# Performance work log

Hardware: AMD Instinct MI355X
Metric: run time of the kernel (lower is better)

The kernel has to match this reference:

```python
import jax, jax.numpy as jnp
import numpy as np

EPS = 1e-5

def _ln(x, g, b):
    mu = jnp.mean(x, axis=-1, keepdims=True)
    var = jnp.var(x, axis=-1, keepdims=True)
    return (x - mu) * jax.lax.rsqrt(var + EPS) * g + b

def setup_inputs() -> dict:
    key = jax.random.key(0)
    ks = jax.random.split(key, 12)
    T, B, D, H = 64, 2048, 512, 512
    seq = jax.random.normal(ks[0], (T, B, D), dtype=jnp.float32)
    ts = jnp.sort(jax.random.uniform(ks[1], (B, T), dtype=jnp.float32) * 10.0, axis=1)
    def xavier(k, shape):
        fan_in, fan_out = shape[1], shape[0]
        lim = float(np.sqrt(6.0 / (fan_in + fan_out)))
        return jax.random.uniform(k, shape, jnp.float32, -lim, lim)
    Wr = xavier(ks[2], (H, D + H)); br = jnp.ones((H,), jnp.float32)   # reset bias init 1.0
    Wz = xavier(ks[3], (H, D + H)); bz = jnp.ones((H,), jnp.float32)   # update bias init 1.0
    Wc = xavier(ks[4], (H, D + H)); bc = jnp.zeros((H,), jnp.float32)
    Wo = xavier(ks[5], (H, H));     bo = jnp.zeros((H,), jnp.float32)  # output projection
    gx = jnp.ones((D,), jnp.float32); bx = jnp.zeros((D,), jnp.float32)  # layer_norm_x
    gh = jnp.ones((H,), jnp.float32); bh = jnp.zeros((H,), jnp.float32)  # layer_norm_h
    gc = jnp.ones((H,), jnp.float32); bcell = jnp.zeros((H,), jnp.float32)  # layer_norm_out (cell)
    gf = jnp.ones((H,), jnp.float32); bf = jnp.zeros((H,), jnp.float32)  # final layer_norm
    return {"seq": seq, "time_stamps": ts,
            "Wr": Wr, "br": br, "Wz": Wz, "bz": bz, "Wc": Wc, "bc": bc,
            "Wo": Wo, "bo": bo, "gx": gx, "bx": bx, "gh": gh, "bh": bh,
            "gc": gc, "bcell": bcell, "gf": gf, "bf": bf}

def _cell(xn, hn, Wr, br, Wz, bz, Wc, bc, gc, bcell):
    # xn: normalized input [B,D]; hn: (normalized, time-scaled) hidden [B,H]
    xh = jnp.concatenate([xn, hn], axis=-1)
    r = jax.nn.sigmoid(xh @ Wr.T + br)
    z = jax.nn.sigmoid(xh @ Wz.T + bz)
    xrh = jnp.concatenate([xn, r * hn], axis=-1)
    h_tilde = jnp.tanh(xrh @ Wc.T + bc)
    h_new = (1.0 - z) * hn + z * h_tilde
    return _ln(h_new, gc, bcell)  # cell output layer norm (dropout is identity in eval)

def reference(seq, time_stamps, Wr, br, Wz, bz, Wc, bc, Wo, bo, gx, bx, gh, bh, gc, bcell, gf, bf):
    T, B, D = seq.shape
    # first step: h is None -> zeros, no LN on h, no time-decay
    x0 = _ln(seq[0], gx, bx)
    h0 = _cell(x0, jnp.zeros((B, Wr.shape[0]), seq.dtype), Wr, br, Wz, bz, Wc, bc, gc, bcell)
    # remaining steps under scan with LN(h) and exp(-dt) decay
    dts = (time_stamps[:, 1:] - time_stamps[:, :-1]).T  # [T-1, B]
    def step(h, inp):
        x_t, dt = inp
        xn = _ln(x_t, gx, bx)
        hn = _ln(h, gh, bh) * jnp.exp(-jnp.clip(dt, 0.0, 10.0))[:, None]
        h_new = _cell(xn, hn, Wr, br, Wz, bz, Wc, bc, gc, bcell)
        return h_new, h_new
    _, rest = jax.lax.scan(step, h0, (seq[1:], dts))
    states = jnp.concatenate([h0[None], rest], axis=0)  # [T,B,H]
    out = jnp.einsum('tbh,oh->tbo', states, Wo) + bo
    out = out + seq  # residual (input_dim == hidden_dim); dropout identity in eval
    return _ln(out, gf, bf)
```

## Files before the change

### kernel.cpp

```cpp
#include <hip/hip_runtime.h>
#include <math.h>

#define TT 64
#define BB 2048

using f32x4   = __attribute__((ext_vector_type(4))) float;
using short8  = __attribute__((ext_vector_type(8))) short;
using short4v = __attribute__((ext_vector_type(4))) short;

__device__ __forceinline__ unsigned short f2bf(float f) {
    unsigned u = __float_as_uint(f);
    u += 0x7FFF + ((u >> 16) & 1);
    return (unsigned short)(u >> 16);
}
__device__ __forceinline__ float bf2f(unsigned short h) {
    return __uint_as_float(((unsigned)h) << 16);
}
__device__ __forceinline__ float sigmoidf_(float v) { return 1.0f / (1.0f + expf(-v)); }
__device__ __forceinline__ float tanhf_(float v)    { return 1.0f - 2.0f / (expf(2.0f * v) + 1.0f); }

__global__ __launch_bounds__(256)
void cvt_kernel(const float* __restrict__ src, unsigned short* __restrict__ dst, int n) {
    int i = blockIdx.x * 256 + threadIdx.x;
    if (i < n) dst[i] = f2bf(src[i]);
}

__global__ __launch_bounds__(256)
void pack_w2(const float* __restrict__ src, unsigned short* __restrict__ dst,
             int N, int Ksrc, int kbeg, int Kpk) {
    int i = blockIdx.x * 256 + threadIdx.x;
    if (i >= N * Kpk) return;
    int n = i / Kpk, k = i - n * Kpk;
    int dstIdx = ((n >> 4) * (Kpk >> 5) + (k >> 5)) * 512 + (((k >> 3) & 3) * 16 + (n & 15)) * 8 + (k & 7);
    dst[dstIdx] = f2bf(src[(size_t)n * Ksrc + kbeg + k]);
}

__device__ __forceinline__ int pk_idx(int row, int col) {
    int ks = col >> 5, khi = (col >> 3) & 3, j = col & 7;
    return ((ks * 64) + khi * 16 + row) * 8 + j;
}

__device__ __forceinline__ void ln_row_pk(const float* __restrict__ xr,
                                          const float* __restrict__ g,
                                          const float* __restrict__ b,
                                          unsigned short* __restrict__ tile,
                                          int row, int lane) {
    const int c0 = lane * 8;
    float4 v0 = *(const float4*)(xr + c0);
    float4 v1 = *(const float4*)(xr + c0 + 4);
    float s  = v0.x + v0.y + v0.z + v0.w + v1.x + v1.y + v1.z + v1.w;
    float ss = v0.x*v0.x + v0.y*v0.y + v0.z*v0.z + v0.w*v0.w
             + v1.x*v1.x + v1.y*v1.y + v1.z*v1.z + v1.w*v1.w;
#pragma unroll
    for (int m = 32; m > 0; m >>= 1) { s += __shfl_xor(s, m); ss += __shfl_xor(ss, m); }
    const float mean = s * (1.0f / 512.0f);
    const float var  = ss * (1.0f / 512.0f) - mean * mean;
    const float rs   = rsqrtf(var + 1e-5f);
    float4 g0 = *(const float4*)(g + c0);
    float4 g1 = *(const float4*)(g + c0 + 4);
    float4 b0 = *(const float4*)(b + c0);
    float4 b1 = *(const float4*)(b + c0 + 4);
    short8 o;
    o[0] = (short)f2bf((v0.x - mean) * rs * g0.x + b0.x);
    o[1] = (short)f2bf((v0.y - mean) * rs * g0.y + b0.y);
    o[2] = (short)f2bf((v0.z - mean) * rs * g0.z + b0.z);
    o[3] = (short)f2bf((v0.w - mean) * rs * g0.w + b0.w);
    o[4] = (short)f2bf((v1.x - mean) * rs * g1.x + b1.x);
    o[5] = (short)f2bf((v1.y - mean) * rs * g1.y + b1.y);
    o[6] = (short)f2bf((v1.z - mean) * rs * g1.z + b1.z);
    o[7] = (short)f2bf((v1.w - mean) * rs * g1.w + b1.w);
    *(short8*)&tile[(((lane >> 2) * 64) + (lane & 3) * 16 + row) * 8] = o;
}

__global__ __launch_bounds__(512)
void gx_kernel(const float* __restrict__ seq, const float* __restrict__ gxw,
               const float* __restrict__ bxw, const unsigned short* __restrict__ Wx3,
               unsigned short* __restrict__ gx)
{
    __shared__ unsigned short xt[4 * 8192];
    const int tid  = threadIdx.x;
    const int w    = tid >> 6;
    const int lane = tid & 63;
    const size_t m0 = (size_t)blockIdx.x * 64;
    const int t    = (int)(m0 >> 11);
    const int bloc = (int)((m0 & 2047) >> 4);

#pragma unroll
    for (int rr = 0; rr < 8; ++rr) {
        const int r = w * 8 + rr;
        ln_row_pk(seq + (m0 + r) * 512, gxw, bxw, xt + (r >> 4) * 8192, r & 15, lane);
    }
    __syncthreads();

    for (int nt = 0; nt < 3; ++nt) {
        f32x4 acc[4][4] = {};
#pragma unroll 4
        for (int ks = 0; ks < 16; ++ks) {
            short8 a[4], b[4];
#pragma unroll
            for (int mf = 0; mf < 4; ++mf)
                a[mf] = *(const short8*)&xt[mf * 8192 + (ks * 64 + lane) * 8];
#pragma unroll
            for (int nf = 0; nf < 4; ++nf)
                b[nf] = *(const short8*)(Wx3 + (size_t)(nt * 32 + w * 4 + nf) * 8192 + ks * 512 + lane * 8);
#pragma unroll
            for (int mf = 0; mf < 4; ++mf)
#pragma unroll
                for (int nf = 0; nf < 4; ++nf)
                    acc[mf][nf] = __builtin_amdgcn_mfma_f32_16x16x32_bf16(a[mf], b[nf], acc[mf][nf], 0, 0, 0);
        }
#pragma unroll
        for (int mf = 0; mf < 4; ++mf)
#pragma unroll
            for (int nf = 0; nf < 4; ++nf) {
                const size_t base = (((size_t)t * 128 + bloc + mf) * 96 + nt * 32 + w * 4 + nf) * 256 + lane * 4;
                short4v o;
                o[0] = (short)f2bf(acc[mf][nf][0]);
                o[1] = (short)f2bf(acc[mf][nf][1]);
                o[2] = (short)f2bf(acc[mf][nf][2]);
                o[3] = (short)f2bf(acc[mf][nf][3]);
                *(short4v*)&gx[base] = o;
            }
    }
}

template<int SBF, int HOIST>
__global__ __launch_bounds__(512)
void recurrent_kernel(const float* __restrict__ seq, const float* __restrict__ ts,
                      const unsigned short* __restrict__ Wrz, const unsigned short* __restrict__ Wc,
                      const float* __restrict__ br, const float* __restrict__ bz,
                      const float* __restrict__ bc,
                      const float* __restrict__ gxw, const float* __restrict__ bxw,
                      const float* __restrict__ gh, const float* __restrict__ bh,
                      const float* __restrict__ gc, const float* __restrict__ bcl,
                      const unsigned short* __restrict__ gx,
                      float* __restrict__ states_f32, unsigned short* __restrict__ states_bf)
{
    __shared__ unsigned short hn_s[16 * 512];
    __shared__ unsigned short rh_s[16 * 512];
    __shared__ unsigned short xn_s[HOIST ? 64 : 16 * 512];
    __shared__ float red_s[16][8];
    __shared__ float red_q[16][8];

    const int tid  = threadIdx.x;
    const int w    = tid >> 6;
    const int lane = tid & 63;
    const int lhi  = lane >> 4;
    const int llo  = lane & 15;
    const int m0   = blockIdx.x * 16;

    for (int i = tid; i < 1024; i += 512) *(short8*)&hn_s[i * 8] = short8{};
    if (!HOIST) {
#pragma unroll
        for (int rr = 0; rr < 2; ++rr) {
            const int r = w * 2 + rr;
            ln_row_pk(seq + (size_t)(m0 + r) * 512, gxw, bxw, xn_s, r, lane);
        }
    }
    __syncthreads();

    float zreg[4][4];

    for (int t = 0; t < TT; ++t) {
        const unsigned short* gxt = HOIST ? gx + (((size_t)t * 128 + blockIdx.x) * 96) * 256 + lane * 4 : nullptr;

        {
            f32x4 aR[4] = {}, aZ[4] = {};
            if (HOIST) {
#pragma unroll
                for (int f = 0; f < 4; ++f) {
                    short4v g1 = *(const short4v*)(gxt + (size_t)(w * 4 + f) * 256);
                    short4v g2 = *(const short4v*)(gxt + (size_t)(32 + w * 4 + f) * 256);
#pragma unroll
                    for (int i = 0; i < 4; ++i) {
                        aR[f][i] = bf2f((unsigned short)g1[i]);
                        aZ[f][i] = bf2f((unsigned short)g2[i]);
                    }
                }
#pragma unroll 4
                for (int ks = 0; ks < 16; ++ks) {
                    short8 a = *(const short8*)&hn_s[(ks * 64 + lane) * 8];
                    const int off = ks * 512 + lane * 8;
#pragma unroll
                    for (int f = 0; f < 4; ++f) {
                        short8 b1 = *(const short8*)(Wrz + (size_t)(w * 4 + f) * 8192 + off);
                        aR[f] = __builtin_amdgcn_mfma_f32_16x16x32_bf16(a, b1, aR[f], 0, 0, 0);
                        short8 b2 = *(const short8*)(Wrz + (size_t)(32 + w * 4 + f) * 8192 + off);
                        aZ[f] = __builtin_amdgcn_mfma_f32_16x16x32_bf16(a, b2, aZ[f], 0, 0, 0);
                    }
                }
            } else {
                const unsigned short* wrb = Wrz + (size_t)(w * 4) * 16384;
                const unsigned short* wzb = Wrz + (size_t)(32 + w * 4) * 16384;
#pragma unroll 4
                for (int ks = 0; ks < 16; ++ks) {
                    short8 a = *(const short8*)&xn_s[(ks * 64 + lane) * 8];
                    const int off = ks * 512 + lane * 8;
#pragma unroll
                    for (int f = 0; f < 4; ++f) {
                        short8 b1 = *(const short8*)(wrb + (size_t)f * 16384 + off);
                        aR[f] = __builtin_amdgcn_mfma_f32_16x16x32_bf16(a, b1, aR[f], 0, 0, 0);
                        short8 b2 = *(const short8*)(wzb + (size_t)f * 16384 + off);
                        aZ[f] = __builtin_amdgcn_mfma_f32_16x16x32_bf16(a, b2, aZ[f], 0, 0, 0);
                    }
                }
#pragma unroll 4
                for (int ks = 16; ks < 32; ++ks) {
                    short8 a = *(const short8*)&hn_s[((ks - 16) * 64 + lane) * 8];
                    const int off = ks * 512 + lane * 8;
#pragma unroll
                    for (int f = 0; f < 4; ++f) {
                        short8 b1 = *(const short8*)(wrb + (size_t)f * 16384 + off);
                        aR[f] = __builtin_amdgcn_mfma_f32_16x16x32_bf16(a, b1, aR[f], 0, 0, 0);
                        short8 b2 = *(const short8*)(wzb + (size_t)f * 16384 + off);
                        aZ[f] = __builtin_amdgcn_mfma_f32_16x16x32_bf16(a, b2, aZ[f], 0, 0, 0);
                    }
                }
            }
#pragma unroll
            for (int f = 0; f < 4; ++f)
#pragma unroll
                for (int i = 0; i < 4; ++i) {
                    const int row = lhi * 4 + i;
                    const int col = w * 64 + f * 16 + llo;
                    const float rr = sigmoidf_(aR[f][i] + br[col]);
                    const float hv = bf2f(hn_s[pk_idx(row, col)]);
                    rh_s[pk_idx(row, col)] = f2bf(rr * hv);
                    zreg[f][i] = sigmoidf_(aZ[f][i] + bz[col]);
                }
        }
        __syncthreads();

        f32x4 aC[4] = {};
        {
            if (HOIST) {
#pragma unroll
                for (int f = 0; f < 4; ++f) {
                    short4v g3 = *(const short4v*)(gxt + (size_t)(64 + w * 4 + f) * 256);
#pragma unroll
                    for (int i = 0; i < 4; ++i) aC[f][i] = bf2f((unsigned short)g3[i]);
                }
#pragma unroll 4
                for (int ks = 0; ks < 16; ++ks) {
                    short8 a = *(const short8*)&rh_s[(ks * 64 + lane) * 8];
                    const int off = ks * 512 + lane * 8;
#pragma unroll
                    for (int f = 0; f < 4; ++f) {
                        short8 b1 = *(const short8*)(Wc + (size_t)(w * 4 + f) * 8192 + off);
                        aC[f] = __builtin_amdgcn_mfma_f32_16x16x32_bf16(a, b1, aC[f], 0, 0, 0);
                    }
                }
            } else {
                const unsigned short* wcb = Wc + (size_t)(w * 4) * 16384;
#pragma unroll 4
                for (int ks = 0; ks < 16; ++ks) {
                    short8 a = *(const short8*)&xn_s[(ks * 64 + lane) * 8];
                    const int off = ks * 512 + lane * 8;
#pragma unroll
                    for (int f = 0; f < 4; ++f) {
                        short8 b1 = *(const short8*)(wcb + (size_t)f * 16384 + off);
                        aC[f] = __builtin_amdgcn_mfma_f32_16x16x32_bf16(a, b1, aC[f], 0, 0, 0);
                    }
                }
#pragma unroll 4
                for (int ks = 16; ks < 32; ++ks) {
                    short8 a = *(const short8*)&rh_s[((ks - 16) * 64 + lane) * 8];
                    const int off = ks * 512 + lane * 8;
#pragma unroll
                    for (int f = 0; f < 4; ++f) {
                        short8 b1 = *(const short8*)(wcb + (size_t)f * 16384 + off);
                        aC[f] = __builtin_amdgcn_mfma_f32_16x16x32_bf16(a, b1, aC[f], 0, 0, 0);
                    }
                }
            }
        }
        __syncthreads();

        {
            float hnew[4][4];
#pragma unroll
            for (int f = 0; f < 4; ++f)
#pragma unroll
                for (int i = 0; i < 4; ++i) {
                    const int row = lhi * 4 + i;
                    const int col = w * 64 + f * 16 + llo;
                    const float htil = tanhf_(aC[f][i] + bc[col]);
                    const float hv = bf2f(hn_s[pk_idx(row, col)]);
                    const float z = zreg[f][i];
                    hnew[f][i] = (1.0f - z) * hv + z * htil;
                }
#pragma unroll
            for (int i = 0; i < 4; ++i) {
                float s = hnew[0][i] + hnew[1][i] + hnew[2][i] + hnew[3][i];
                float q = hnew[0][i]*hnew[0][i] + hnew[1][i]*hnew[1][i]
                        + hnew[2][i]*hnew[2][i] + hnew[3][i]*hnew[3][i];
#pragma unroll
                for (int m = 8; m >= 1; m >>= 1) { s += __shfl_xor(s, m); q += __shfl_xor(q, m); }
                if (llo == 0) { red_s[lhi * 4 + i][w] = s; red_q[lhi * 4 + i][w] = q; }
            }
            __syncthreads();
            float mu[4], rsd[4];
#pragma unroll
            for (int i = 0; i < 4; ++i) {
                float s = 0.f, q = 0.f;
#pragma unroll
                for (int w2 = 0; w2 < 8; ++w2) { s += red_s[lhi * 4 + i][w2]; q += red_q[lhi * 4 + i][w2]; }
                const float m_ = s * (1.0f / 512.0f);
                mu[i]  = m_;
                rsd[i] = rsqrtf(q * (1.0f / 512.0f) - m_ * m_ + 1e-5f);
            }
#pragma unroll
            for (int f = 0; f < 4; ++f)
#pragma unroll
                for (int i = 0; i < 4; ++i) {
                    const int row = lhi * 4 + i;
                    const int col = w * 64 + f * 16 + llo;
                    const float h = (hnew[f][i] - mu[i]) * rsd[i] * gc[col] + bcl[col];
                    const size_t off = (size_t)t * BB * 512 + (size_t)(m0 + row) * 512 + col;
                    if (SBF) states_bf[off] = f2bf(h);
                    else     states_f32[off] = h;
                    hnew[f][i] = h;
                }
            if (t + 1 < TT) {
                __syncthreads();
#pragma unroll
                for (int i = 0; i < 4; ++i) {
                    float s = hnew[0][i] + hnew[1][i] + hnew[2][i] + hnew[3][i];
                    float q = hnew[0][i]*hnew[0][i] + hnew[1][i]*hnew[1][i]
                            + hnew[2][i]*hnew[2][i] + hnew[3][i]*hnew[3][i];
#pragma unroll
                    for (int m = 8; m >= 1; m >>= 1) { s += __shfl_xor(s, m); q += __shfl_xor(q, m); }
                    if (llo == 0) { red_s[lhi * 4 + i][w] = s; red_q[lhi * 4 + i][w] = q; }
                }
                __syncthreads();
                float dec_[4];
#pragma unroll
                for (int i = 0; i < 4; ++i) {
                    float s = 0.f, q = 0.f;
#pragma unroll
                    for (int w2 = 0; w2 < 8; ++w2) { s += red_s[lhi * 4 + i][w2]; q += red_q[lhi * 4 + i][w2]; }
                    const float m_ = s * (1.0f / 512.0f);
                    mu[i]  = m_;
                    rsd[i] = rsqrtf(q * (1.0f / 512.0f) - m_ * m_ + 1e-5f);
                    const int row = m0 + lhi * 4 + i;
                    float dtv = ts[(size_t)row * TT + t + 1] - ts[(size_t)row * TT + t];
                    dtv = fminf(fmaxf(dtv, 0.0f), 10.0f);
                    dec_[i] = expf(-dtv);
                }
#pragma unroll
                for (int f = 0; f < 4; ++f)
#pragma unroll
                    for (int i = 0; i < 4; ++i) {
                        const int row = lhi * 4 + i;
                        const int col = w * 64 + f * 16 + llo;
                        const float hv = ((hnew[f][i] - mu[i]) * rsd[i] * gh[col] + bh[col]) * dec_[i];
                        hn_s[pk_idx(row, col)] = f2bf(hv);
                    }
                if (!HOIST) {
#pragma unroll
                    for (int rr = 0; rr < 2; ++rr) {
                        const int r = w * 2 + rr;
                        ln_row_pk(seq + ((size_t)(t + 1) * BB + m0 + r) * 512, gxw, bxw, xn_s, r, lane);
                    }
                }
            }
        }
        __syncthreads();
    }
}

template<int BF>
__global__ __launch_bounds__(512)
void proj_kernel(const float* __restrict__ S, const unsigned short* __restrict__ Sb,
                 const unsigned short* __restrict__ Wo, const float* __restrict__ bo,
                 const float* __restrict__ seq, const float* __restrict__ gf,
                 const float* __restrict__ bff, float* __restrict__ out)
{
    const int tid  = threadIdx.x;
    const int wave = tid >> 6;
    const int lane = tid & 63;
    const int lhi  = lane >> 4;
    const int llo  = lane & 15;
    const long m0  = (long)blockIdx.x * 64;

    f32x4 acc[4][4] = {};
    for (int k0 = 0; k0 < 512; k0 += 32) {
        const int kk = k0 + lhi * 8;
        short8 a[4], b[4];
#pragma unroll
        for (int mf = 0; mf < 4; ++mf) {
            if (BF) {
                a[mf] = *(const short8*)(Sb + (size_t)(m0 + mf * 16 + llo) * 512 + kk);
            } else {
                const float* ap = S + (size_t)(m0 + mf * 16 + llo) * 512 + kk;
                float4 f0 = *(const float4*)ap;
                float4 f1 = *(const float4*)(ap + 4);
                short8 av;
                av[0] = (short)f2bf(f0.x); av[1] = (short)f2bf(f0.y);
                av[2] = (short)f2bf(f0.z); av[3] = (short)f2bf(f0.w);
                av[4] = (short)f2bf(f1.x); av[5] = (short)f2bf(f1.y);
                av[6] = (short)f2bf(f1.z); av[7] = (short)f2bf(f1.w);
                a[mf] = av;
            }
        }
#pragma unroll
        for (int nf = 0; nf < 4; ++nf)
            b[nf] = *(const short8*)(Wo + (size_t)(wave * 64 + nf * 16 + llo) * 512 + kk);
#pragma unroll
        for (int mf = 0; mf < 4; ++mf)
#pragma unroll
            for (int nf = 0; nf < 4; ++nf)
                acc[mf][nf] = __builtin_amdgcn_mfma_f32_16x16x32_bf16(a[mf], b[nf], acc[mf][nf], 0, 0, 0);
    }

    __shared__ float red_s[64][8];
    __shared__ float red_q[64][8];

#pragma unroll
    for (int mf = 0; mf < 4; ++mf)
#pragma unroll
        for (int i = 0; i < 4; ++i) {
            const long row = m0 + mf * 16 + lhi * 4 + i;
#pragma unroll
            for (int nf = 0; nf < 4; ++nf) {
                const int col = wave * 64 + nf * 16 + llo;
                acc[mf][nf][i] += bo[col] + seq[(size_t)row * 512 + col];
            }
        }
    float mu[4][4], rstd[4][4];
#pragma unroll
    for (int mf = 0; mf < 4; ++mf)
#pragma unroll
        for (int i = 0; i < 4; ++i) {
            float s = 0.f, q = 0.f;
#pragma unroll
            for (int nf = 0; nf < 4; ++nf) { const float v = acc[mf][nf][i]; s += v; q += v * v; }
#pragma unroll
            for (int m = 8; m >= 1; m >>= 1) { s += __shfl_xor(s, m); q += __shfl_xor(q, m); }
            if (llo == 0) { red_s[mf * 16 + lhi * 4 + i][wave] = s; red_q[mf * 16 + lhi * 4 + i][wave] = q; }
        }
    __syncthreads();
#pragma unroll
    for (int mf = 0; mf < 4; ++mf)
#pragma unroll
        for (int i = 0; i < 4; ++i) {
            const int rl = mf * 16 + lhi * 4 + i;
            float s = 0.f, q = 0.f;
#pragma unroll
            for (int w2 = 0; w2 < 8; ++w2) { s += red_s[rl][w2]; q += red_q[rl][w2]; }
            const float m_ = s * (1.0f / 512.0f);
            const float var = q * (1.0f / 512.0f) - m_ * m_;
            mu[mf][i] = m_;
            rstd[mf][i] = rsqrtf(var + 1e-5f);
        }
#pragma unroll
    for (int mf = 0; mf < 4; ++mf)
#pragma unroll
        for (int i = 0; i < 4; ++i) {
            const long row = m0 + mf * 16 + lhi * 4 + i;
#pragma unroll
            for (int nf = 0; nf < 4; ++nf) {
                const int col = wave * 64 + nf * 16 + llo;
                out[(size_t)row * 512 + col] = (acc[mf][nf][i] - mu[mf][i]) * rstd[mf][i] * gf[col] + bff[col];
            }
        }
}

extern "C" void kernel_launch(void* const* d_in, const int* in_sizes, int n_in,
                              void* d_out, int out_size, void* d_ws, size_t ws_size,
                              hipStream_t stream) {
    const float* seq = (const float*)d_in[0];
    const float* ts  = (const float*)d_in[1];
    const float* Wr  = (const float*)d_in[2];
    const float* br  = (const float*)d_in[3];
    const float* Wz  = (const float*)d_in[4];
    const float* bz  = (const float*)d_in[5];
    const float* Wc  = (const float*)d_in[6];
    const float* bc  = (const float*)d_in[7];
    const float* Wo  = (const float*)d_in[8];
    const float* bo  = (const float*)d_in[9];
    const float* gx  = (const float*)d_in[10];
    const float* bx  = (const float*)d_in[11];
    const float* gh  = (const float*)d_in[12];
    const float* bh  = (const float*)d_in[13];
    const float* gc  = (const float*)d_in[14];
    const float* bcl = (const float*)d_in[15];
    const float* gf  = (const float*)d_in[16];
    const float* bf  = (const float*)d_in[17];
    float* out = (float*)d_out;

    char* w0 = (char*)d_ws;
    char* w = w0;
    unsigned short* Wrz_full = (unsigned short*)w; w += (size_t)1024 * 1024 * 2;
    unsigned short* Wc_full  = (unsigned short*)w; w += (size_t)512 * 1024 * 2;
    unsigned short* Wrz_h    = (unsigned short*)w; w += (size_t)1024 * 512 * 2;
    unsigned short* Wc_h     = (unsigned short*)w; w += (size_t)512 * 512 * 2;
    unsigned short* Wx3      = (unsigned short*)w; w += (size_t)1536 * 512 * 2;
    unsigned short* Wo_b     = (unsigned short*)w; w += (size_t)512 * 512 * 2;

    const size_t GXB = (size_t)TT * 128 * 96 * 256 * 2;
    const size_t SBB = (size_t)TT * BB * 512 * 2;

    const bool hoist = ws_size >= (size_t)(w - w0) + GXB;
    unsigned short* gxbuf = (unsigned short*)w;
    if (hoist) w += GXB;
    const bool sbf = ws_size >= (size_t)(w - w0) + SBB;
    unsigned short* states_bf = (unsigned short*)w;

    if (hoist) {
        pack_w2<<<1024, 256, 0, stream>>>(Wr, Wrz_h, 512, 1024, 512, 512);
        pack_w2<<<1024, 256, 0, stream>>>(Wz, Wrz_h + (size_t)512 * 512, 512, 1024, 512, 512);
        pack_w2<<<1024, 256, 0, stream>>>(Wc, Wc_h, 512, 1024, 512, 512);
        pack_w2<<<1024, 256, 0, stream>>>(Wr, Wx3, 512, 1024, 0, 512);
        pack_w2<<<1024, 256, 0, stream>>>(Wz, Wx3 + (size_t)512 * 512, 512, 1024, 0, 512);
        pack_w2<<<1024, 256, 0, stream>>>(Wc, Wx3 + (size_t)2 * 512 * 512, 512, 1024, 0, 512);
    } else {
        pack_w2<<<2048, 256, 0, stream>>>(Wr, Wrz_full, 512, 1024, 0, 1024);
        pack_w2<<<2048, 256, 0, stream>>>(Wz, Wrz_full + (size_t)512 * 1024, 512, 1024, 0, 1024);
        pack_w2<<<2048, 256, 0, stream>>>(Wc, Wc_full, 512, 1024, 0, 1024);
    }
    cvt_kernel<<<(512 * 512 + 255) / 256, 256, 0, stream>>>(Wo, Wo_b, 512 * 512);

    if (hoist)
        gx_kernel<<<2048, 512, 0, stream>>>(seq, gx, bx, Wx3, gxbuf);

    const unsigned short* Wa = hoist ? Wrz_h : Wrz_full;
    const unsigned short* Wb = hoist ? Wc_h  : Wc_full;
    if (hoist) {
        if (sbf) recurrent_kernel<1,1><<<128, 512, 0, stream>>>(seq, ts, Wa, Wb, br, bz, bc, gx, bx, gh, bh, gc, bcl, gxbuf, out, states_bf);
        else     recurrent_kernel<0,1><<<128, 512, 0, stream>>>(seq, ts, Wa, Wb, br, bz, bc, gx, bx, gh, bh, gc, bcl, gxbuf, out, states_bf);
    } else {
        if (sbf) recurrent_kernel<1,0><<<128, 512, 0, stream>>>(seq, ts, Wa, Wb, br, bz, bc, gx, bx, gh, bh, gc, bcl, gxbuf, out, states_bf);
        else     recurrent_kernel<0,0><<<128, 512, 0, stream>>>(seq, ts, Wa, Wb, br, bz, bc, gx, bx, gh, bh, gc, bcl, gxbuf, out, states_bf);
    }

    if (sbf)
        proj_kernel<1><<<2048, 512, 0, stream>>>(out, states_bf, Wo_b, bo, seq, gf, bf, out);
    else
        proj_kernel<0><<<2048, 512, 0, stream>>>(out, nullptr, Wo_b, bo, seq, gf, bf, out);
}
```

Measured before the change: 1.877 ms.

## Store bf16 states and Wo in MFMA-packed layout for contiguous projection loads

The recurrent kernel now writes bf16 hidden states in a per-block, MFMA-fragment-packed layout, and Wo is packed the same way with pack_w2 instead of a plain conversion. The projection kernel can then load each A and B fragment as one contiguous 16-byte read per lane instead of strided row reads. This targets memory coalescing in the output projection. Smaller changes ride along: the non-hoisted GEMM loops are merged, the z-gate reuses the aR registers, and the reduction arrays are padded to avoid bank conflicts. These add register-pressure and layout-consistency risk.

```diff
diff --git a/kernel.cpp b/kernel.cpp
--- a/kernel.cpp
+++ b/kernel.cpp
@@ -18,12 +18,6 @@
 }
 __device__ __forceinline__ float sigmoidf_(float v) { return 1.0f / (1.0f + expf(-v)); }
 __device__ __forceinline__ float tanhf_(float v)    { return 1.0f - 2.0f / (expf(2.0f * v) + 1.0f); }
-
-__global__ __launch_bounds__(256)
-void cvt_kernel(const float* __restrict__ src, unsigned short* __restrict__ dst, int n) {
-    int i = blockIdx.x * 256 + threadIdx.x;
-    if (i < n) dst[i] = f2bf(src[i]);
-}
 
 __global__ __launch_bounds__(256)
 void pack_w2(const float* __restrict__ src, unsigned short* __restrict__ dst,
@@ -134,13 +128,13 @@
                       const float* __restrict__ gh, const float* __restrict__ bh,
                       const float* __restrict__ gc, const float* __restrict__ bcl,
                       const unsigned short* __restrict__ gx,
-                      float* __restrict__ states_f32, unsigned short* __restrict__ states_bf)
+                      float* __restrict__ states_f32, unsigned short* __restrict__ states_pk)
 {
     __shared__ unsigned short hn_s[16 * 512];
     __shared__ unsigned short rh_s[16 * 512];
     __shared__ unsigned short xn_s[HOIST ? 64 : 16 * 512];
-    __shared__ float red_s[16][8];
-    __shared__ float red_q[16][8];
+    __shared__ float red_s[16][9];
+    __shared__ float red_q[16][9];
 
     const int tid  = threadIdx.x;
     const int w    = tid >> 6;
@@ -159,13 +153,11 @@
     }
     __syncthreads();
 
-    float zreg[4][4];
-
     for (int t = 0; t < TT; ++t) {
         const unsigned short* gxt = HOIST ? gx + (((size_t)t * 128 + blockIdx.x) * 96) * 256 + lane * 4 : nullptr;
 
         {
-            f32x4 aR[4] = {}, aZ[4] = {};
+            f32x4 aR[4], aZ[4];
             if (HOIST) {
 #pragma unroll
                 for (int f = 0; f < 4; ++f) {
@@ -190,29 +182,18 @@
                     }
                 }
             } else {
-                const unsigned short* wrb = Wrz + (size_t)(w * 4) * 16384;
-                const unsigned short* wzb = Wrz + (size_t)(32 + w * 4) * 16384;
-#pragma unroll 4
-                for (int ks = 0; ks < 16; ++ks) {
-                    short8 a = *(const short8*)&xn_s[(ks * 64 + lane) * 8];
+#pragma unroll
+                for (int f = 0; f < 4; ++f) { aR[f] = f32x4{}; aZ[f] = f32x4{}; }
+#pragma unroll 2
+                for (int ks = 0; ks < 32; ++ks) {
+                    short8 a = (ks < 16) ? *(const short8*)&xn_s[(ks * 64 + lane) * 8]
+                                         : *(const short8*)&hn_s[((ks - 16) * 64 + lane) * 8];
                     const int off = ks * 512 + lane * 8;
 #pragma unroll
                     for (int f = 0; f < 4; ++f) {
-                        short8 b1 = *(const short8*)(wrb + (size_t)f * 16384 + off);
+                        short8 b1 = *(const short8*)(Wrz + (size_t)(w * 4 + f) * 16384 + off);
                         aR[f] = __builtin_amdgcn_mfma_f32_16x16x32_bf16(a, b1, aR[f], 0, 0, 0);
-                        short8 b2 = *(const short8*)(wzb + (size_t)f * 16384 + off);
-                        aZ[f] = __builtin_amdgcn_mfma_f32_16x16x32_bf16(a, b2, aZ[f], 0, 0, 0);
-                    }
-                }
-#pragma unroll 4
-                for (int ks = 16; ks < 32; ++ks) {
-                    short8 a = *(const short8*)&hn_s[((ks - 16) * 64 + lane) * 8];
-                    const int off = ks * 512 + lane * 8;
-#pragma unroll
-                    for (int f = 0; f < 4; ++f) {
-                        short8 b1 = *(const short8*)(wrb + (size_t)f * 16384 + off);
-                        aR[f] = __builtin_amdgcn_mfma_f32_16x16x32_bf16(a, b1, aR[f], 0, 0, 0);
-                        short8 b2 = *(const short8*)(wzb + (size_t)f * 16384 + off);
+                        short8 b2 = *(const short8*)(Wrz + (size_t)(32 + w * 4 + f) * 16384 + off);
                         aZ[f] = __builtin_amdgcn_mfma_f32_16x16x32_bf16(a, b2, aZ[f], 0, 0, 0);
                     }
                 }
@@ -226,13 +207,11 @@
                     const float rr = sigmoidf_(aR[f][i] + br[col]);
                     const float hv = bf2f(hn_s[pk_idx(row, col)]);
                     rh_s[pk_idx(row, col)] = f2bf(rr * hv);
-                    zreg[f][i] = sigmoidf_(aZ[f][i] + bz[col]);
-                }
-        }
-        __syncthreads();
-
-        f32x4 aC[4] = {};
-        {
+                    aR[f][i] = sigmoidf_(aZ[f][i] + bz[col]);
+                }
+            __syncthreads();
+
+            f32x4 aC[4];
             if (HOIST) {
 #pragma unroll
                 for (int f = 0; f < 4; ++f) {
@@ -251,32 +230,22 @@
                     }
                 }
             } else {
-                const unsigned short* wcb = Wc + (size_t)(w * 4) * 16384;
-#pragma unroll 4
-                for (int ks = 0; ks < 16; ++ks) {
-                    short8 a = *(const short8*)&xn_s[(ks * 64 + lane) * 8];
+#pragma unroll
+                for (int f = 0; f < 4; ++f) aC[f] = f32x4{};
+#pragma unroll 2
+                for (int ks = 0; ks < 32; ++ks) {
+                    short8 a = (ks < 16) ? *(const short8*)&xn_s[(ks * 64 + lane) * 8]
+                                         : *(const short8*)&rh_s[((ks - 16) * 64 + lane) * 8];
                     const int off = ks * 512 + lane * 8;
 #pragma unroll
                     for (int f = 0; f < 4; ++f) {
-                        short8 b1 = *(const short8*)(wcb + (size_t)f * 16384 + off);
+                        short8 b1 = *(const short8*)(Wc + (size_t)(w * 4 + f) * 16384 + off);
                         aC[f] = __builtin_amdgcn_mfma_f32_16x16x32_bf16(a, b1, aC[f], 0, 0, 0);
                     }
                 }
-#pragma unroll 4
-                for (int ks = 16; ks < 32; ++ks) {
-                    short8 a = *(const short8*)&rh_s[((ks - 16) * 64 + lane) * 8];
-                    const int off = ks * 512 + lane * 8;
-#pragma unroll
-                    for (int f = 0; f < 4; ++f) {
-                        short8 b1 = *(const short8*)(wcb + (size_t)f * 16384 + off);
-                        aC[f] = __builtin_amdgcn_mfma_f32_16x16x32_bf16(a, b1, aC[f], 0, 0, 0);
-                    }
-                }
-            }
-        }
-        __syncthreads();
-
-        {
+            }
+            __syncthreads();
+
             float hnew[4][4];
 #pragma unroll
             for (int f = 0; f < 4; ++f)
@@ -286,7 +255,7 @@
                     const int col = w * 64 + f * 16 + llo;
                     const float htil = tanhf_(aC[f][i] + bc[col]);
                     const float hv = bf2f(hn_s[pk_idx(row, col)]);
-                    const float z = zreg[f][i];
+                    const float z = aR[f][i];
                     hnew[f][i] = (1.0f - z) * hv + z * htil;
                 }
 #pragma unroll
@@ -316,9 +285,8 @@
                     const int row = lhi * 4 + i;
                     const int col = w * 64 + f * 16 + llo;
                     const float h = (hnew[f][i] - mu[i]) * rsd[i] * gc[col] + bcl[col];
-                    const size_t off = (size_t)t * BB * 512 + (size_t)(m0 + row) * 512 + col;
-                    if (SBF) states_bf[off] = f2bf(h);
-                    else     states_f32[off] = h;
+                    if (SBF) states_pk[((size_t)t * 128 + blockIdx.x) * 8192 + pk_idx(row, col)] = f2bf(h);
+                    else     states_f32[(size_t)t * BB * 512 + (size_t)(m0 + row) * 512 + col] = h;
                     hnew[f][i] = h;
                 }
             if (t + 1 < TT) {
@@ -342,8 +310,8 @@
                     const float m_ = s * (1.0f / 512.0f);
                     mu[i]  = m_;
                     rsd[i] = rsqrtf(q * (1.0f / 512.0f) - m_ * m_ + 1e-5f);
-                    const int row = m0 + lhi * 4 + i;
-                    float dtv = ts[(size_t)row * TT + t + 1] - ts[(size_t)row * TT + t];
+                    const int grow = m0 + lhi * 4 + i;
+                    float dtv = ts[(size_t)grow * TT + t + 1] - ts[(size_t)grow * TT + t];
                     dtv = fminf(fmaxf(dtv, 0.0f), 10.0f);
                     dec_[i] = expf(-dtv);
                 }
@@ -371,7 +339,7 @@
 
 template<int BF>
 __global__ __launch_bounds__(512)
-void proj_kernel(const float* __restrict__ S, const unsigned short* __restrict__ Sb,
+void proj_kernel(const float* __restrict__ S, const unsigned short* __restrict__ Spk,
                  const unsigned short* __restrict__ Wo, const float* __restrict__ bo,
                  const float* __restrict__ seq, const float* __restrict__ gf,
                  const float* __restrict__ bff, float* __restrict__ out)
@@ -382,17 +350,19 @@
     const int lhi  = lane >> 4;
     const int llo  = lane & 15;
     const long m0  = (long)blockIdx.x * 64;
+    const int t    = (int)(m0 >> 11);
+    const int blk  = (int)((m0 & 2047) >> 4);
 
     f32x4 acc[4][4] = {};
-    for (int k0 = 0; k0 < 512; k0 += 32) {
-        const int kk = k0 + lhi * 8;
+#pragma unroll 2
+    for (int ks = 0; ks < 16; ++ks) {
         short8 a[4], b[4];
 #pragma unroll
         for (int mf = 0; mf < 4; ++mf) {
             if (BF) {
-                a[mf] = *(const short8*)(Sb + (size_t)(m0 + mf * 16 + llo) * 512 + kk);
+                a[mf] = *(const short8*)(Spk + ((size_t)t * 128 + blk + mf) * 8192 + (ks * 64 + lane) * 8);
             } else {
-                const float* ap = S + (size_t)(m0 + mf * 16 + llo) * 512 + kk;
+                const float* ap = S + (size_t)(m0 + mf * 16 + llo) * 512 + ks * 32 + lhi * 8;
                 float4 f0 = *(const float4*)ap;
                 float4 f1 = *(const float4*)(ap + 4);
                 short8 av;
@@ -405,7 +375,7 @@
         }
 #pragma unroll
         for (int nf = 0; nf < 4; ++nf)
-            b[nf] = *(const short8*)(Wo + (size_t)(wave * 64 + nf * 16 + llo) * 512 + kk);
+            b[nf] = *(const short8*)(Wo + (size_t)(wave * 4 + nf) * 8192 + ks * 512 + lane * 8);
 #pragma unroll
         for (int mf = 0; mf < 4; ++mf)
 #pragma unroll
@@ -413,8 +383,8 @@
                 acc[mf][nf] = __builtin_amdgcn_mfma_f32_16x16x32_bf16(a[mf], b[nf], acc[mf][nf], 0, 0, 0);
     }
 
-    __shared__ float red_s[64][8];
-    __shared__ float red_q[64][8];
+    __shared__ float red_s[64][9];
+    __shared__ float red_q[64][9];
 
 #pragma unroll
     for (int mf = 0; mf < 4; ++mf)
@@ -449,9 +419,8 @@
 #pragma unroll
             for (int w2 = 0; w2 < 8; ++w2) { s += red_s[rl][w2]; q += red_q[rl][w2]; }
             const float m_ = s * (1.0f / 512.0f);
-            const float var = q * (1.0f / 512.0f) - m_ * m_;
             mu[mf][i] = m_;
-            rstd[mf][i] = rsqrtf(var + 1e-5f);
+            rstd[mf][i] = rsqrtf(q * (1.0f / 512.0f) - m_ * m_ + 1e-5f);
         }
 #pragma unroll
     for (int mf = 0; mf < 4; ++mf)
@@ -496,16 +465,16 @@
     unsigned short* Wrz_h    = (unsigned short*)w; w += (size_t)1024 * 512 * 2;
     unsigned short* Wc_h     = (unsigned short*)w; w += (size_t)512 * 512 * 2;
     unsigned short* Wx3      = (unsigned short*)w; w += (size_t)1536 * 512 * 2;
-    unsigned short* Wo_b     = (unsigned short*)w; w += (size_t)512 * 512 * 2;
+    unsigned short* Wo_pk    = (unsigned short*)w; w += (size_t)512 * 512 * 2;
 
     const size_t GXB = (size_t)TT * 128 * 96 * 256 * 2;
-    const size_t SBB = (size_t)TT * BB * 512 * 2;
+    const size_t SBB = (size_t)TT * 128 * 8192 * 2;
 
     const bool hoist = ws_size >= (size_t)(w - w0) + GXB;
     unsigned short* gxbuf = (unsigned short*)w;
     if (hoist) w += GXB;
     const bool sbf = ws_size >= (size_t)(w - w0) + SBB;
-    unsigned short* states_bf = (unsigned short*)w;
+    unsigned short* states_pk = (unsigned short*)w;
 
     if (hoist) {
         pack_w2<<<1024, 256, 0, stream>>>(Wr, Wrz_h, 512, 1024, 512, 512);
@@ -519,7 +488,7 @@
         pack_w2<<<2048, 256, 0, stream>>>(Wz, Wrz_full + (size_t)512 * 1024, 512, 1024, 0, 1024);
         pack_w2<<<2048, 256, 0, stream>>>(Wc, Wc_full, 512, 1024, 0, 1024);
     }
-    cvt_kernel<<<(512 * 512 + 255) / 256, 256, 0, stream>>>(Wo, Wo_b, 512 * 512);
+    pack_w2<<<1024, 256, 0, stream>>>(Wo, Wo_pk, 512, 512, 0, 512);
 
     if (hoist)
         gx_kernel<<<2048, 512, 0, stream>>>(seq, gx, bx, Wx3, gxbuf);
@@ -527,15 +496,15 @@
     const unsigned short* Wa = hoist ? Wrz_h : Wrz_full;
     const unsigned short* Wb = hoist ? Wc_h  : Wc_full;
     if (hoist) {
-        if (sbf) recurrent_kernel<1,1><<<128, 512, 0, stream>>>(seq, ts, Wa, Wb, br, bz, bc, gx, bx, gh, bh, gc, bcl, gxbuf, out, states_bf);
-        else     recurrent_kernel<0,1><<<128, 512, 0, stream>>>(seq, ts, Wa, Wb, br, bz, bc, gx, bx, gh, bh, gc, bcl, gxbuf, out, states_bf);
+        if (sbf) recurrent_kernel<1,1><<<128, 512, 0, stream>>>(seq, ts, Wa, Wb, br, bz, bc, gx, bx, gh, bh, gc, bcl, gxbuf, out, states_pk);
+        else     recurrent_kernel<0,1><<<128, 512, 0, stream>>>(seq, ts, Wa, Wb, br, bz, bc, gx, bx, gh, bh, gc, bcl, gxbuf, out, states_pk);
     } else {
-        if (sbf) recurrent_kernel<1,0><<<128, 512, 0, stream>>>(seq, ts, Wa, Wb, br, bz, bc, gx, bx, gh, bh, gc, bcl, gxbuf, out, states_bf);
-        else     recurrent_kernel<0,0><<<128, 512, 0, stream>>>(seq, ts, Wa, Wb, br, bz, bc, gx, bx, gh, bh, gc, bcl, gxbuf, out, states_bf);
+        if (sbf) recurrent_kernel<1,0><<<128, 512, 0, stream>>>(seq, ts, Wa, Wb, br, bz, bc, gx, bx, gh, bh, gc, bcl, gxbuf, out, states_pk);
+        else     recurrent_kernel<0,0><<<128, 512, 0, stream>>>(seq, ts, Wa, Wb, br, bz, bc, gx, bx, gh, bh, gc, bcl, gxbuf, out, states_pk);
     }
 
     if (sbf)
-        proj_kernel<1><<<2048, 512, 0, stream>>>(out, states_bf, Wo_b, bo, seq, gf, bf, out);
+        proj_kernel<1><<<2048, 512, 0, stream>>>(nullptr, states_pk, Wo_pk, bo, seq, gf, bf, out);
     else
-        proj_kernel<0><<<2048, 512, 0, stream>>>(out, nullptr, Wo_b, bo, seq, gf, bf, out);
-}
+        proj_kernel<0><<<2048, 512, 0, stream>>>(out, nullptr, Wo_pk, bo, seq, gf, bf, out);
+}
```

Result: faster. 1.792 ms (-4.5%).
